# Optimization experiments

Measured on AMD Instinct MI355X. Metric: run time of the kernel, lower is better.

The kernel has to match this reference:

```python
import jax, jax.numpy as jnp
import numpy as np

B, T, C = 4, 2048, 2048
H, HKV = 16, 4
D = C // H            # 128
G = H // HKV          # 4 query heads per kv head
ROPE_THETA = 10000.0


def _rope_tables(seq_len, head_dim, theta):
    inv = 1.0 / (theta ** (np.arange(0, head_dim, 2, dtype=np.float32) / head_dim))
    t = np.arange(seq_len, dtype=np.float32)
    f = np.outer(t, inv)  # (T, D/2)
    return jnp.asarray(np.cos(f)), jnp.asarray(np.sin(f))


def setup_inputs() -> dict:
    key = jax.random.key(0)
    ks = jax.random.split(key, 5)
    x = jax.random.normal(ks[0], (B, T, C), dtype=jnp.float32)
    W_q = jax.random.normal(ks[1], (H * D, C), dtype=jnp.float32) * 0.02
    W_k = jax.random.normal(ks[2], (HKV * D, C), dtype=jnp.float32) * 0.02
    W_v = jax.random.normal(ks[3], (HKV * D, C), dtype=jnp.float32) * 0.02
    W_o = jax.random.normal(ks[4], (C, C), dtype=jnp.float32) * 0.02
    cos, sin = _rope_tables(T, D, ROPE_THETA)
    return {"x": x, "W_q": W_q, "W_k": W_k, "W_v": W_v, "W_o": W_o,
            "cos": cos, "sin": sin}


def _apply_rope(xh, cos, sin):
    # xh: (B, h, T, D); cos/sin: (T, D/2)
    x0 = xh[..., 0::2]
    x1 = xh[..., 1::2]
    c = cos[None, None, :, :]
    s = sin[None, None, :, :]
    o0 = x0 * c - x1 * s
    o1 = x0 * s + x1 * c
    return jnp.stack([o0, o1], axis=-1).reshape(xh.shape)


def reference(x, W_q, W_k, W_v, W_o, cos, sin):
    b, t, c = x.shape
    q = (x @ W_q.T).reshape(b, t, H, D).transpose(0, 2, 1, 3)      # (B,H,T,D)
    k = (x @ W_k.T).reshape(b, t, HKV, D).transpose(0, 2, 1, 3)    # (B,HKV,T,D)
    v = (x @ W_v.T).reshape(b, t, HKV, D).transpose(0, 2, 1, 3)
    q = _apply_rope(q, cos[:t], sin[:t])
    k = _apply_rope(k, cos[:t], sin[:t])
    # GQA via reshape instead of repeat_interleave (same head ordering:
    # q head index h = kv*G + g).
    qg = q.reshape(b, HKV, G, t, D)
    scores = jnp.einsum('bkgtd,bksd->bkgts', qg, k) / jnp.sqrt(jnp.float32(D))
    causal = jnp.tril(jnp.ones((t, t), dtype=bool))
    scores = jnp.where(causal[None, None, None, :, :], scores, -jnp.inf)
    attn = jax.nn.softmax(scores, axis=-1)
    out = jnp.einsum('bkgts,bksd->bkgtd', attn, v)                 # (B,HKV,G,T,D)
    out = out.reshape(b, H, t, D).transpose(0, 2, 1, 3).reshape(b, t, c)
    return out @ W_o.T
```

## Files before the change

kernel.cpp:

```cpp
#include <hip/hip_runtime.h>
#include <cmath>

typedef __attribute__((ext_vector_type(8))) short bf16x8;
typedef __attribute__((ext_vector_type(4))) float f32x4;
typedef __attribute__((ext_vector_type(16))) float f32x16;
typedef unsigned short u16;

__device__ __forceinline__ u16 f2bf(float f) {
  union { float f; unsigned u; } x; x.f = f;
  return (u16)((x.u + 0x7FFFu + ((x.u >> 16) & 1u)) >> 16);
}

__device__ __forceinline__ unsigned cvtpk(float lo, float hi) {
  unsigned r;
  asm("v_cvt_pk_bf16_f32 %0, %1, %2" : "=v"(r) : "v"(lo), "v"(hi));
  return r;
}

__device__ __forceinline__ void gload_lds16(const void* g, void* l) {
  __builtin_amdgcn_global_load_lds((const __attribute__((address_space(1))) unsigned*)g,
                                   (__attribute__((address_space(3))) unsigned*)l,
                                   16, 0, 0);
}

__global__ __launch_bounds__(256) void cast_all_kernel(const float* __restrict__ x,
                                                       const float* __restrict__ wq,
                                                       const float* __restrict__ wk,
                                                       const float* __restrict__ wv,
                                                       const float* __restrict__ wo,
                                                       u16* __restrict__ out) {
  const long b1 = 16777216, b2 = 20971520, b3 = 22020096, b4 = 23068672, b5 = 27262976;
  long i = (long)blockIdx.x * blockDim.x + threadIdx.x;
  long stride = (long)gridDim.x * blockDim.x;
  for (long j = i * 4; j < b5; j += stride * 4) {
    const float* src; long off;
    if (j < b1)      { src = x;  off = j; }
    else if (j < b2) { src = wq; off = j - b1; }
    else if (j < b3) { src = wk; off = j - b2; }
    else if (j < b4) { src = wv; off = j - b3; }
    else             { src = wo; off = j - b4; }
    float4 v = *(const float4*)(src + off);
    ushort4 o;
    o.x = f2bf(v.x); o.y = f2bf(v.y); o.z = f2bf(v.z); o.w = f2bf(v.w);
    *(ushort4*)(out + j) = o;
  }
}

template <int EPI>
__global__ __launch_bounds__(512, 2) void gemm_bt256(const u16* __restrict__ A,
                                                     const u16* __restrict__ B,
                                                     void* __restrict__ outp,
                                                     int M, int N, int K,
                                                     const float* __restrict__ cosp,
                                                     const float* __restrict__ sinp,
                                                     float scale) {
  __shared__ u16 lds[65536];
  const int tid = threadIdx.x;
  const int lane = tid & 63;
  const int l16 = lane & 15, lhi = lane >> 4;
  const int w = tid >> 6;
  const int wr = w >> 2, wc = w & 3;
  const int m0 = blockIdx.y * 256;
  const int n0 = blockIdx.x * 256;

  f32x4 acc[8][4];
#pragma unroll
  for (int i = 0; i < 8; ++i)
#pragma unroll
    for (int j = 0; j < 4; ++j) acc[i][j] = (f32x4)0.0f;

  const int NT = K >> 6;

  auto stage = [&](int t, int buf) {
    const int k0 = t << 6;
    u16* Ad = lds + buf * 32768;
    u16* Bd = Ad + 16384;
#pragma unroll
    for (int j = 0; j < 4; ++j) {
      int c = tid + j * 512;
      int row = c >> 3;
      int sboff = ((c & 7) * 16) ^ ((row & 7) << 4);
      gload_lds16(A + (size_t)(m0 + row) * K + k0 + (sboff >> 1), Ad + (size_t)c * 8);
    }
#pragma unroll
    for (int j = 0; j < 4; ++j) {
      int c = tid + j * 512;
      int row = c >> 3;
      int sboff = ((c & 7) * 16) ^ ((row & 7) << 4);
      gload_lds16(B + (size_t)(n0 + row) * K + k0 + (sboff >> 1), Bd + (size_t)c * 8);
    }
  };

  stage(0, 0);
  stage(1, 1);

  for (int t = 0; t < NT; ++t) {
    const int cur = t & 1;
    if (t + 1 < NT) { asm volatile("s_waitcnt vmcnt(8)" ::: "memory"); }
    else            { asm volatile("s_waitcnt vmcnt(0)" ::: "memory"); }
    __builtin_amdgcn_s_barrier();
    const char* Ab = (const char*)(lds + cur * 32768);
    const char* Bb = (const char*)(lds + cur * 32768 + 16384);
#pragma unroll
    for (int qm = 0; qm < 2; ++qm)
#pragma unroll
      for (int qn = 0; qn < 2; ++qn) {
        bf16x8 af[4][2], bfr[2][2];
#pragma unroll
        for (int mi = 0; mi < 4; ++mi) {
          int ra = wr * 128 + qm * 64 + mi * 16 + l16;
#pragma unroll
          for (int kk = 0; kk < 2; ++kk)
            af[mi][kk] = *(const bf16x8*)(Ab + ra * 128 + ((kk * 64 + lhi * 16) ^ ((ra & 7) << 4)));
        }
#pragma unroll
        for (int ni = 0; ni < 2; ++ni) {
          int rb = wc * 64 + qn * 32 + ni * 16 + l16;
#pragma unroll
          for (int kk = 0; kk < 2; ++kk)
            bfr[ni][kk] = *(const bf16x8*)(Bb + rb * 128 + ((kk * 64 + lhi * 16) ^ ((rb & 7) << 4)));
        }
        __builtin_amdgcn_s_setprio(1);
#pragma unroll
        for (int kk = 0; kk < 2; ++kk)
#pragma unroll
          for (int mi = 0; mi < 4; ++mi)
#pragma unroll
            for (int ni = 0; ni < 2; ++ni)
              acc[qm * 4 + mi][qn * 2 + ni] = __builtin_amdgcn_mfma_f32_16x16x32_bf16(
                  af[mi][kk], bfr[ni][kk], acc[qm * 4 + mi][qn * 2 + ni], 0, 0, 0);
        __builtin_amdgcn_s_setprio(0);
      }
    asm volatile("s_waitcnt lgkmcnt(0)" ::: "memory");
    __builtin_amdgcn_s_barrier();
    if (t + 2 < NT) stage(t + 2, cur);
  }

  if (EPI == 2) {
    float* o = (float*)outp;
#pragma unroll
    for (int mi8 = 0; mi8 < 8; ++mi8)
#pragma unroll
      for (int r = 0; r < 4; ++r) {
        int row = m0 + wr * 128 + mi8 * 16 + lhi * 4 + r;
#pragma unroll
        for (int nj = 0; nj < 4; ++nj) {
          int col = n0 + wc * 64 + nj * 16 + l16;
          o[(size_t)row * N + col] = acc[mi8][nj][r];
        }
      }
  } else {
    u16* o = (u16*)outp;
    const int nheads = N >> 7;
#pragma unroll
    for (int mi8 = 0; mi8 < 8; ++mi8)
#pragma unroll
      for (int r = 0; r < 4; ++r) {
        int row = m0 + wr * 128 + mi8 * 16 + lhi * 4 + r;
        int b = row >> 11;
        int tt = row & 2047;
#pragma unroll
        for (int nj = 0; nj < 4; ++nj) {
          int col = n0 + wc * 64 + nj * 16 + l16;
          int hh = col >> 7, dd = col & 127;
          float v = acc[mi8][nj][r];
          float p = __shfl_xor(v, 1);
          float c = cosp[tt * 64 + (dd >> 1)];
          float s = sinp[tt * 64 + (dd >> 1)];
          v = (lane & 1) ? fmaf(p, s, v * c) : fmaf(v, c, -p * s);
          v *= scale;
          o[((size_t)(b * nheads + hh) * 2048 + tt) * 128 + dd] = f2bf(v);
        }
      }
  }
}

template <int EPI>
__global__ __launch_bounds__(256) void gemm_bt(const u16* __restrict__ A,
                                               const u16* __restrict__ B,
                                               void* __restrict__ outp,
                                               u16* __restrict__ vtp,
                                               int M, int N, int K,
                                               const float* __restrict__ cosp,
                                               const float* __restrict__ sinp,
                                               float scale) {
  __shared__ u16 As[128 * 64];
  __shared__ u16 Bs[128 * 64];
  const int tid = threadIdx.x;
  const int lane = tid & 63;
  const int l16 = lane & 15, lhi = lane >> 4;
  const int w = tid >> 6;
  const int wr = w >> 1, wc = w & 1;
  const int m0 = blockIdx.y * 128;
  const int n0 = blockIdx.x * 128;
  const int wbase = tid - lane;

  f32x4 acc[4][4];
#pragma unroll
  for (int i = 0; i < 4; ++i)
#pragma unroll
    for (int j = 0; j < 4; ++j) acc[i][j] = (f32x4)0.0f;

  for (int k0 = 0; k0 < K; k0 += 64) {
    __syncthreads();
#pragma unroll
    for (int j = 0; j < 4; ++j) {
      int c = tid + j * 256;
      gload_lds16(A + (size_t)(m0 + (c >> 3)) * K + k0 + (c & 7) * 8,
                  As + (size_t)(wbase + j * 256) * 8);
    }
#pragma unroll
    for (int j = 0; j < 4; ++j) {
      int c = tid + j * 256;
      gload_lds16(B + (size_t)(n0 + (c >> 3)) * K + k0 + (c & 7) * 8,
                  Bs + (size_t)(wbase + j * 256) * 8);
    }
    __syncthreads();
#pragma unroll
    for (int kk = 0; kk < 64; kk += 32) {
      bf16x8 af[4], bfr[4];
#pragma unroll
      for (int mi = 0; mi < 4; ++mi)
        af[mi] = *(const bf16x8*)&As[(wr * 64 + mi * 16 + l16) * 64 + kk + lhi * 8];
#pragma unroll
      for (int ni = 0; ni < 4; ++ni)
        bfr[ni] = *(const bf16x8*)&Bs[(wc * 64 + ni * 16 + l16) * 64 + kk + lhi * 8];
#pragma unroll
      for (int mi = 0; mi < 4; ++mi)
#pragma unroll
        for (int ni = 0; ni < 4; ++ni)
          acc[mi][ni] = __builtin_amdgcn_mfma_f32_16x16x32_bf16(af[mi], bfr[ni], acc[mi][ni], 0, 0, 0);
    }
  }

  {
    const int bx = blockIdx.x;
    if (bx < 4) {
      u16* o = (u16*)outp;
#pragma unroll
      for (int mi = 0; mi < 4; ++mi)
#pragma unroll
        for (int r = 0; r < 4; ++r) {
          int row = m0 + wr * 64 + mi * 16 + lhi * 4 + r;
          int b = row >> 11;
          int t = row & 2047;
          size_t base = ((size_t)(b * 4 + bx) * 2048 + t) * 128;
#pragma unroll
          for (int ni = 0; ni < 4; ++ni) {
            int d = wc * 64 + ni * 16 + l16;
            float v = acc[mi][ni][r];
            float p = __shfl_xor(v, 1);
            float c = cosp[t * 64 + (d >> 1)];
            float s = sinp[t * 64 + (d >> 1)];
            v = (lane & 1) ? fmaf(p, s, v * c) : fmaf(v, c, -p * s);
            o[base + d] = f2bf(v);
          }
        }
    } else {
      const int kvh = bx - 4;
#pragma unroll
      for (int mi = 0; mi < 4; ++mi)
#pragma unroll
        for (int r = 0; r < 4; ++r) {
          int row = m0 + wr * 64 + mi * 16 + lhi * 4 + r;
          int b = row >> 11;
          int t = row & 2047;
          size_t base = ((size_t)(b * 4 + kvh) * 128) * 2048 + t;
#pragma unroll
          for (int ni = 0; ni < 4; ++ni) {
            int d = wc * 64 + ni * 16 + l16;
            vtp[base + (size_t)d * 2048] = f2bf(acc[mi][ni][r]);
          }
        }
    }
  }
}

__global__ __launch_bounds__(512, 2) void attn_kernel(const u16* __restrict__ Q,
                                                      const u16* __restrict__ Kp,
                                                      const u16* __restrict__ Vtp,
                                                      u16* __restrict__ O) {
  __shared__ u16 lds[32768];

  const int tid = threadIdx.x;
  const int lane = tid & 63;
  const int w = tid >> 6;
  const int l5 = lane & 31, hi = lane >> 5;
  const int bid = blockIdx.x;
  const int qt = 7 - (bid >> 6);
  const int hb = bid & 63;
  const int h = hb >> 2;
  const int b = hb & 3;
  const int kvh = h >> 2;
  const int q0 = qt * 256;
  const int wbase = tid - lane;
  const int wrow0 = q0 + w * 32;
  const int qg = wrow0 + l5;

  const u16* Qb = Q + ((size_t)((b * 16 + h) * 2048 + wrow0)) * 128;
  const u16* Kb = Kp + (size_t)(b * 4 + kvh) * 2048 * 128;
  const u16* Vtb = Vtp + (size_t)(b * 4 + kvh) * 128 * 2048;

  bf16x8 qf[8];
#pragma unroll
  for (int ks = 0; ks < 8; ++ks)
    qf[ks] = *(const bf16x8*)(Qb + (size_t)l5 * 128 + ks * 16 + hi * 8);

  f32x16 oacc[4];
#pragma unroll
  for (int i = 0; i < 4; ++i) oacc[i] = (f32x16)0.0f;
  float m = -3.0e38f, l = 0.0f;

  const int nkt = 4 * qt + 4;

  auto stageKV = [&](int kt, int buf) {
    const int t0k = kt * 64;
    u16* Kd = lds + buf * 8192;
    u16* Vd = lds + 16384 + buf * 8192;
#pragma unroll
    for (int j = 0; j < 2; ++j) {
      int c = tid + j * 512;
      int row = c >> 4;
      int sboff = ((c & 15) * 16) ^ ((row & 15) << 4);
      gload_lds16(Kb + (size_t)(t0k + row) * 128 + (sboff >> 1),
                  Kd + (size_t)(wbase + j * 512) * 8);
    }
#pragma unroll
    for (int j = 0; j < 2; ++j) {
      int c = tid + j * 512;
      int d = c >> 3;
      int sboff = ((c & 7) * 16) ^ ((d & 7) << 4);
      gload_lds16(Vtb + (size_t)d * 2048 + t0k + (sboff >> 1),
                  Vd + (size_t)(wbase + j * 512) * 8);
    }
  };

  stageKV(0, 0);

  for (int kt = 0; kt < nkt; ++kt) {
    const int t0 = kt * 64;
    const int cur = kt & 1;
    if (kt + 1 < nkt) {
      stageKV(kt + 1, cur ^ 1);
      asm volatile("s_waitcnt vmcnt(4)" ::: "memory");
    } else {
      asm volatile("s_waitcnt vmcnt(0)" ::: "memory");
    }
    __builtin_amdgcn_s_barrier();

    if (t0 <= wrow0 + 31) {
      const char* ksb = (const char*)(lds + cur * 8192);
      const char* vtb = (const char*)(lds + 16384 + cur * 8192);

      float p[32];
#pragma unroll
      for (int kt2 = 0; kt2 < 2; ++kt2) {
        f32x16 sacc = (f32x16)0.0f;
        int row = kt2 * 32 + l5;
        __builtin_amdgcn_s_setprio(1);
#pragma unroll
        for (int ks = 0; ks < 8; ++ks) {
          bf16x8 kf = *(const bf16x8*)(ksb + row * 256 + ((ks * 32 + hi * 16) ^ ((row & 15) << 4)));
          sacc = __builtin_amdgcn_mfma_f32_32x32x16_bf16(kf, qf[ks], sacc, 0, 0, 0);
        }
        __builtin_amdgcn_s_setprio(0);
#pragma unroll
        for (int r = 0; r < 16; ++r) p[kt2 * 16 + r] = sacc[r];
      }

      if (t0 + 63 > wrow0) {
#pragma unroll
        for (int kt2 = 0; kt2 < 2; ++kt2)
#pragma unroll
          for (int r = 0; r < 16; ++r) {
            int kvg = t0 + kt2 * 32 + (r & 3) + 8 * (r >> 2) + 4 * hi;
            if (kvg > qg) p[kt2 * 16 + r] = -3.0e38f;
          }
      }

      float mx[16];
#pragma unroll
      for (int i = 0; i < 16; ++i) mx[i] = fmaxf(p[i], p[i + 16]);
#pragma unroll
      for (int i = 0; i < 8; ++i) mx[i] = fmaxf(mx[i], mx[i + 8]);
#pragma unroll
      for (int i = 0; i < 4; ++i) mx[i] = fmaxf(mx[i], mx[i + 4]);
      float rm = fmaxf(fmaxf(mx[0], mx[1]), fmaxf(mx[2], mx[3]));
      rm = fmaxf(rm, __shfl_xor(rm, 32));

      bool defer = __all(rm <= m + 8.0f);
      if (!defer) {
        float mnew = fmaxf(m, rm);
        float sc = exp2f(m - mnew);
        m = mnew;
        l *= sc;
#pragma unroll
        for (int i = 0; i < 4; ++i)
#pragma unroll
          for (int r = 0; r < 16; ++r) oacc[i][r] *= sc;
      }

#pragma unroll
      for (int i = 0; i < 32; ++i) p[i] = exp2f(p[i] - m);
      float sm[16];
#pragma unroll
      for (int i = 0; i < 16; ++i) sm[i] = p[i] + p[i + 16];
#pragma unroll
      for (int i = 0; i < 8; ++i) sm[i] += sm[i + 8];
#pragma unroll
      for (int i = 0; i < 4; ++i) sm[i] += sm[i + 4];
      float s2 = (sm[0] + sm[1]) + (sm[2] + sm[3]);
      s2 += __shfl_xor(s2, 32);
      l += s2;

#pragma unroll
      for (int kt2 = 0; kt2 < 2; ++kt2) {
#pragma unroll
        for (int sl = 0; sl < 2; ++sl) {
          int base = kt2 * 16 + sl * 8;
          unsigned A0 = cvtpk(p[base + 0], p[base + 1]);
          unsigned A1 = cvtpk(p[base + 2], p[base + 3]);
          unsigned A2 = cvtpk(p[base + 4], p[base + 5]);
          unsigned A3 = cvtpk(p[base + 6], p[base + 7]);
          asm volatile("v_permlane32_swap_b32 %0, %1" : "+v"(A0), "+v"(A2));
          asm volatile("v_permlane32_swap_b32 %0, %1" : "+v"(A1), "+v"(A3));
          union { unsigned u[4]; bf16x8 v; } pf;
          pf.u[0] = A0;
          pf.u[1] = A1;
          pf.u[2] = A2;
          pf.u[3] = A3;
          int s = kt2 * 2 + sl;
          __builtin_amdgcn_s_setprio(1);
#pragma unroll
          for (int dt = 0; dt < 4; ++dt) {
            int row = dt * 32 + l5;
            bf16x8 vb = *(const bf16x8*)(vtb + row * 128 + ((s * 32 + hi * 16) ^ ((row & 7) << 4)));
            oacc[dt] = __builtin_amdgcn_mfma_f32_32x32x16_bf16(vb, pf.v, oacc[dt], 0, 0, 0);
          }
          __builtin_amdgcn_s_setprio(0);
        }
      }
    }

    asm volatile("s_waitcnt lgkmcnt(0)" ::: "memory");
    __builtin_amdgcn_s_barrier();
  }

  float inv = 1.0f / l;
  __syncthreads();
  for (int half = 0; half < 2; ++half) {
    if ((w >> 2) == half) {
      u16* OSw = lds + (w & 3) * 4352;
#pragma unroll
      for (int dt = 0; dt < 4; ++dt)
#pragma unroll
        for (int r = 0; r < 16; ++r) {
          int d = dt * 32 + (r & 3) + 8 * (r >> 2) + 4 * hi;
          OSw[l5 * 136 + d] = f2bf(oacc[dt][r] * inv);
        }
    }
    __syncthreads();
    u16* Ob = O + ((size_t)(b * 2048 + q0 + half * 128)) * 2048 + h * 128;
#pragma unroll
    for (int j = 0; j < 4; ++j) {
      int c = tid + j * 512;
      int row = c >> 4, col = c & 15;
      *(bf16x8*)(Ob + (size_t)row * 2048 + col * 8) =
          *(const bf16x8*)&lds[(row >> 5) * 4352 + (row & 31) * 136 + col * 8];
    }
    __syncthreads();
  }
}

extern "C" void kernel_launch(void* const* d_in, const int* in_sizes, int n_in,
                              void* d_out, int out_size, void* d_ws, size_t ws_size,
                              hipStream_t stream) {
  (void)in_sizes; (void)n_in; (void)out_size; (void)ws_size;
  const float* x    = (const float*)d_in[0];
  const float* Wq   = (const float*)d_in[1];
  const float* Wk   = (const float*)d_in[2];
  const float* Wv   = (const float*)d_in[3];
  const float* Wo   = (const float*)d_in[4];
  const float* cosp = (const float*)d_in[5];
  const float* sinp = (const float*)d_in[6];

  u16* ws  = (u16*)d_ws;
  u16* xbf = ws;
  u16* Wqb = xbf + 16777216;
  u16* Wkb = Wqb + 4194304;
  u16* Wvb = Wkb + 1048576;
  u16* Wob = Wvb + 1048576;
  u16* Qb  = Wob + 4194304;
  u16* Kb  = Qb + 16777216;
  u16* Vb  = Kb + 4194304;
  u16* AO  = xbf;

  cast_all_kernel<<<2048, 256, 0, stream>>>(x, Wq, Wk, Wv, Wo, ws);

  const float qscale = (float)(1.4426950408889634 / sqrt(128.0));

  gemm_bt256<0><<<dim3(8, 32), 512, 0, stream>>>(xbf, Wqb, Qb, 8192, 2048, 2048, cosp, sinp, qscale);
  gemm_bt<3><<<dim3(8, 64), 256, 0, stream>>>(xbf, Wkb, Kb, Vb, 8192, 1024, 2048, cosp, sinp, 1.0f);

  attn_kernel<<<512, 512, 0, stream>>>(Qb, Kb, Vb, AO);

  gemm_bt256<2><<<dim3(8, 32), 512, 0, stream>>>(AO, Wob, d_out, 8192, 2048, 2048, nullptr, nullptr, 1.0f);
}
```

Before: 341.3 us.

## Fuse Q, K and V projections into one 256-tile GEMM launch

Replaces the separate Q projection GEMM and the 128-tile K/V GEMM with a single gemm_bt256 launch over N=3072. This relies on Wq, Wk and Wv being stored back to back in the workspace. The epilogue branches per block on the column range: RoPE plus scale for Q, RoPE for K, and a transposed store for V. The aim is to drop one kernel launch and move the K/V work onto the larger, more efficient tile kernel, so the whole QKV projection runs as one grid. The cost is a larger epilogue with per-block branching.

```diff
diff --git a/kernel.cpp b/kernel.cpp
--- a/kernel.cpp
+++ b/kernel.cpp
@@ -50,6 +50,8 @@
 __global__ __launch_bounds__(512, 2) void gemm_bt256(const u16* __restrict__ A,
                                                      const u16* __restrict__ B,
                                                      void* __restrict__ outp,
+                                                     u16* __restrict__ kp,
+                                                     u16* __restrict__ vtp,
                                                      int M, int N, int K,
                                                      const float* __restrict__ cosp,
                                                      const float* __restrict__ sinp,
@@ -150,8 +152,7 @@
         }
       }
   } else {
-    u16* o = (u16*)outp;
-    const int nheads = N >> 7;
+    u16* oq = (u16*)outp;
 #pragma unroll
     for (int mi8 = 0; mi8 < 8; ++mi8)
 #pragma unroll
@@ -162,117 +163,29 @@
 #pragma unroll
         for (int nj = 0; nj < 4; ++nj) {
           int col = n0 + wc * 64 + nj * 16 + l16;
-          int hh = col >> 7, dd = col & 127;
           float v = acc[mi8][nj][r];
-          float p = __shfl_xor(v, 1);
-          float c = cosp[tt * 64 + (dd >> 1)];
-          float s = sinp[tt * 64 + (dd >> 1)];
-          v = (lane & 1) ? fmaf(p, s, v * c) : fmaf(v, c, -p * s);
-          v *= scale;
-          o[((size_t)(b * nheads + hh) * 2048 + tt) * 128 + dd] = f2bf(v);
-        }
-      }
-  }
-}
-
-template <int EPI>
-__global__ __launch_bounds__(256) void gemm_bt(const u16* __restrict__ A,
-                                               const u16* __restrict__ B,
-                                               void* __restrict__ outp,
-                                               u16* __restrict__ vtp,
-                                               int M, int N, int K,
-                                               const float* __restrict__ cosp,
-                                               const float* __restrict__ sinp,
-                                               float scale) {
-  __shared__ u16 As[128 * 64];
-  __shared__ u16 Bs[128 * 64];
-  const int tid = threadIdx.x;
-  const int lane = tid & 63;
-  const int l16 = lane & 15, lhi = lane >> 4;
-  const int w = tid >> 6;
-  const int wr = w >> 1, wc = w & 1;
-  const int m0 = blockIdx.y * 128;
-  const int n0 = blockIdx.x * 128;
-  const int wbase = tid - lane;
-
-  f32x4 acc[4][4];
-#pragma unroll
-  for (int i = 0; i < 4; ++i)
-#pragma unroll
-    for (int j = 0; j < 4; ++j) acc[i][j] = (f32x4)0.0f;
-
-  for (int k0 = 0; k0 < K; k0 += 64) {
-    __syncthreads();
-#pragma unroll
-    for (int j = 0; j < 4; ++j) {
-      int c = tid + j * 256;
-      gload_lds16(A + (size_t)(m0 + (c >> 3)) * K + k0 + (c & 7) * 8,
-                  As + (size_t)(wbase + j * 256) * 8);
-    }
-#pragma unroll
-    for (int j = 0; j < 4; ++j) {
-      int c = tid + j * 256;
-      gload_lds16(B + (size_t)(n0 + (c >> 3)) * K + k0 + (c & 7) * 8,
-                  Bs + (size_t)(wbase + j * 256) * 8);
-    }
-    __syncthreads();
-#pragma unroll
-    for (int kk = 0; kk < 64; kk += 32) {
-      bf16x8 af[4], bfr[4];
-#pragma unroll
-      for (int mi = 0; mi < 4; ++mi)
-        af[mi] = *(const bf16x8*)&As[(wr * 64 + mi * 16 + l16) * 64 + kk + lhi * 8];
-#pragma unroll
-      for (int ni = 0; ni < 4; ++ni)
-        bfr[ni] = *(const bf16x8*)&Bs[(wc * 64 + ni * 16 + l16) * 64 + kk + lhi * 8];
-#pragma unroll
-      for (int mi = 0; mi < 4; ++mi)
-#pragma unroll
-        for (int ni = 0; ni < 4; ++ni)
-          acc[mi][ni] = __builtin_amdgcn_mfma_f32_16x16x32_bf16(af[mi], bfr[ni], acc[mi][ni], 0, 0, 0);
-    }
-  }
-
-  {
-    const int bx = blockIdx.x;
-    if (bx < 4) {
-      u16* o = (u16*)outp;
-#pragma unroll
-      for (int mi = 0; mi < 4; ++mi)
-#pragma unroll
-        for (int r = 0; r < 4; ++r) {
-          int row = m0 + wr * 64 + mi * 16 + lhi * 4 + r;
-          int b = row >> 11;
-          int t = row & 2047;
-          size_t base = ((size_t)(b * 4 + bx) * 2048 + t) * 128;
-#pragma unroll
-          for (int ni = 0; ni < 4; ++ni) {
-            int d = wc * 64 + ni * 16 + l16;
-            float v = acc[mi][ni][r];
+          if (n0 < 2048) {
+            int dd = col & 127;
             float p = __shfl_xor(v, 1);
-            float c = cosp[t * 64 + (d >> 1)];
-            float s = sinp[t * 64 + (d >> 1)];
+            float c = cosp[tt * 64 + (dd >> 1)];
+            float s = sinp[tt * 64 + (dd >> 1)];
             v = (lane & 1) ? fmaf(p, s, v * c) : fmaf(v, c, -p * s);
-            o[base + d] = f2bf(v);
+            v *= scale;
+            oq[((size_t)(b * 16 + (col >> 7)) * 2048 + tt) * 128 + dd] = f2bf(v);
+          } else if (n0 < 2560) {
+            int c2 = col - 2048;
+            int dd = c2 & 127;
+            float p = __shfl_xor(v, 1);
+            float c = cosp[tt * 64 + (dd >> 1)];
+            float s = sinp[tt * 64 + (dd >> 1)];
+            v = (lane & 1) ? fmaf(p, s, v * c) : fmaf(v, c, -p * s);
+            kp[((size_t)(b * 4 + (c2 >> 7)) * 2048 + tt) * 128 + dd] = f2bf(v);
+          } else {
+            int c2 = col - 2560;
+            vtp[((size_t)(b * 4 + (c2 >> 7)) * 128 + (c2 & 127)) * 2048 + tt] = f2bf(v);
           }
         }
-    } else {
-      const int kvh = bx - 4;
-#pragma unroll
-      for (int mi = 0; mi < 4; ++mi)
-#pragma unroll
-        for (int r = 0; r < 4; ++r) {
-          int row = m0 + wr * 64 + mi * 16 + lhi * 4 + r;
-          int b = row >> 11;
-          int t = row & 2047;
-          size_t base = ((size_t)(b * 4 + kvh) * 128) * 2048 + t;
-#pragma unroll
-          for (int ni = 0; ni < 4; ++ni) {
-            int d = wc * 64 + ni * 16 + l16;
-            vtp[base + (size_t)d * 2048] = f2bf(acc[mi][ni][r]);
-          }
-        }
-    }
+      }
   }
 }
 
@@ -499,10 +412,11 @@
 
   const float qscale = (float)(1.4426950408889634 / sqrt(128.0));
 
-  gemm_bt256<0><<<dim3(8, 32), 512, 0, stream>>>(xbf, Wqb, Qb, 8192, 2048, 2048, cosp, sinp, qscale);
-  gemm_bt<3><<<dim3(8, 64), 256, 0, stream>>>(xbf, Wkb, Kb, Vb, 8192, 1024, 2048, cosp, sinp, 1.0f);
+  gemm_bt256<1><<<dim3(12, 32), 512, 0, stream>>>(xbf, Wqb, Qb, Kb, Vb,
+                                                  8192, 3072, 2048, cosp, sinp, qscale);
 
   attn_kernel<<<512, 512, 0, stream>>>(Qb, Kb, Vb, AO);
 
-  gemm_bt256<2><<<dim3(8, 32), 512, 0, stream>>>(AO, Wob, d_out, 8192, 2048, 2048, nullptr, nullptr, 1.0f);
-}
+  gemm_bt256<2><<<dim3(8, 32), 512, 0, stream>>>(AO, Wob, d_out, nullptr, nullptr,
+                                                 8192, 2048, 2048, nullptr, nullptr, 1.0f);
+}
```

Result: slower. 375.3 us (+10.0%).
